# Optimization experiments

Measured on AMD Instinct MI355X. Metric: run time of the kernel, lower is better.

## Reference

```python
import jax, jax.numpy as jnp
import numpy as np
from jax import lax

B, S, TW = 16, 128, 16
VOCAB, EDIM = 50000, 300
NCHARS, CEDIM, CH = 100, 50, 50
HID = 256
NTAGS, MAXR = 10, 16
H2 = 2 * HID


def _lstm_dir(x, mask, wih, whh, b):
    # x: [N,T,D], mask: [N,T] bool. Returns masked outputs [N,T,H] and final hidden [N,H].
    Hd = whh.shape[1]
    Nn = x.shape[0]

    def step(carry, inp):
        h, c = carry
        xt, m = inp  # xt [N,D], m [N,1]
        z = xt @ wih.T + h @ whh.T + b
        i, f, g, o = jnp.split(z, 4, axis=-1)
        c_new = jax.nn.sigmoid(f) * c + jax.nn.sigmoid(i) * jnp.tanh(g)
        h_new = jax.nn.sigmoid(o) * jnp.tanh(c_new)
        c = jnp.where(m, c_new, c)
        h = jnp.where(m, h_new, h)
        return (h, c), jnp.where(m, h_new, 0.0)

    h0 = jnp.zeros((Nn, Hd), x.dtype)
    (hn, _), ys = lax.scan(step, (h0, h0), (x.transpose(1, 0, 2), mask.T[..., None]))
    return ys.transpose(1, 0, 2), hn


def _bilstm(x, lengths, pf, pb):
    # Mirrors pack_padded_sequence -> LSTM -> pad_packed (zeros past length).
    T = x.shape[1]
    mask = jnp.arange(T)[None, :] < lengths[:, None]
    yf, hf = _lstm_dir(x, mask, *pf)
    # per-sequence reversal for the backward direction
    idx = jnp.maximum(lengths[:, None] - 1 - jnp.arange(T)[None, :], 0)
    xr = jnp.take_along_axis(x, idx[:, :, None], axis=1)
    ybr, hb = _lstm_dir(xr, mask, *pb)
    yb = jnp.take_along_axis(ybr, idx[:, :, None], axis=1) * mask[:, :, None]
    return jnp.concatenate([yf, yb], -1), jnp.concatenate([hf, hb], -1)


def _forward(emb, char_emb, c_wih_f, c_whh_f, c_b_f, c_wih_b, c_whh_b, c_b_b,
             w_wih_f, w_whh_f, w_b_f, w_wih_b, w_whh_b, w_b_b, clf_w, clf_b,
             sentences, sentence_lengths, word_chars, word_lengths):
    word_repr = emb[sentences]  # [B,S,EDIM]
    # CharLSTM: final bi-hidden per word (all words of all sentences batched)
    cw = word_chars.reshape(B * S, TW)
    cl = word_lengths.reshape(B * S)
    ce = char_emb[cw]  # [B*S,TW,CEDIM]
    _, hn = _bilstm(ce, cl, (c_wih_f, c_whh_f, c_b_f), (c_wih_b, c_whh_b, c_b_b))
    sent_mask = jnp.arange(S)[None, :] < sentence_lengths[:, None]
    char_feat = hn.reshape(B, S, 2 * CH) * sent_mask[:, :, None]  # pad_sequence zeros
    x = jnp.concatenate([word_repr, char_feat], -1)  # [B,S,400]
    out, _ = _bilstm(x, sentence_lengths, (w_wih_f, w_whh_f, w_b_f), (w_wih_b, w_whh_b, w_b_b))
    u = out.transpose(1, 0, 2)  # [S,B,2H]  (unpacked.transpose(0,1))
    # prefix sums collapse the exhaustive sliding-window means into one pass
    csum = jnp.concatenate([jnp.zeros((1, B, H2), u.dtype), jnp.cumsum(u, axis=0)], 0)
    starts = np.concatenate([np.arange(0, S - r + 1) for r in range(1, MAXR + 1)])
    sizes = np.concatenate([np.full(S - r + 1, r) for r in range(1, MAXR + 1)])
    first = u[starts]                                   # [N,B,2H]
    last = u[starts + sizes - 1]                        # [N,B,2H]
    mean = (csum[starts + sizes] - csum[starts]) / jnp.asarray(sizes, u.dtype)[:, None, None]
    feats = jnp.concatenate([first, mean, last], -1)    # [N,B,6H]
    logits = jax.nn.relu(feats) @ clf_w.T + clf_b       # [N,B,NTAGS]
    return logits.transpose(1, 2, 0)                    # [B,NTAGS,N] (stack dim=-1)


def setup_inputs() -> dict:
    key = jax.random.key(0)
    ks = jax.random.split(key, 12)
    sc = 0.08

    def lstm_p(k, D, Hd):
        k1, k2, k3 = jax.random.split(k, 3)
        return (jax.random.normal(k1, (4 * Hd, D), jnp.float32) * sc,
                jax.random.normal(k2, (4 * Hd, Hd), jnp.float32) * sc,
                jax.random.normal(k3, (4 * Hd,), jnp.float32) * sc)

    emb = (jax.random.normal(ks[0], (VOCAB, EDIM), jnp.float32) * sc).at[0].set(0.0)
    char_emb = (jax.random.normal(ks[1], (NCHARS, CEDIM), jnp.float32) * sc).at[0].set(0.0)
    c_wih_f, c_whh_f, c_b_f = lstm_p(ks[2], CEDIM, CH)
    c_wih_b, c_whh_b, c_b_b = lstm_p(ks[3], CEDIM, CH)
    w_wih_f, w_whh_f, w_b_f = lstm_p(ks[4], EDIM + 2 * CH, HID)
    w_wih_b, w_whh_b, w_b_b = lstm_p(ks[5], EDIM + 2 * CH, HID)
    clf_w = jax.random.normal(ks[6], (NTAGS, 3 * H2), jnp.float32) * sc
    clf_b = jax.random.normal(ks[7], (NTAGS,), jnp.float32) * sc

    sentences = jax.random.randint(ks[8], (B, S), 1, VOCAB, jnp.int32)
    sl = jnp.sort(jax.random.randint(ks[9], (B,), S // 2, S + 1, jnp.int32))[::-1]
    sentence_lengths = sl.at[0].set(S)  # descending; max_len = S (static)
    word_chars = jax.random.randint(ks[10], (B, S, TW), 1, NCHARS, jnp.int32)
    word_lengths = jax.random.randint(ks[11], (B, S), 1, TW + 1, jnp.int32)

    return dict(emb=emb, char_emb=char_emb,
                c_wih_f=c_wih_f, c_whh_f=c_whh_f, c_b_f=c_b_f,
                c_wih_b=c_wih_b, c_whh_b=c_whh_b, c_b_b=c_b_b,
                w_wih_f=w_wih_f, w_whh_f=w_whh_f, w_b_f=w_b_f,
                w_wih_b=w_wih_b, w_whh_b=w_whh_b, w_b_b=w_b_b,
                clf_w=clf_w, clf_b=clf_b,
                sentences=sentences, sentence_lengths=sentence_lengths,
                word_chars=word_chars, word_lengths=word_lengths)


def reference(emb, char_emb, c_wih_f, c_whh_f, c_b_f, c_wih_b, c_whh_b, c_b_b,
              w_wih_f, w_whh_f, w_b_f, w_wih_b, w_whh_b, w_b_b, clf_w, clf_b,
              sentences, sentence_lengths, word_chars, word_lengths):
    return _forward(emb, char_emb, c_wih_f, c_whh_f, c_b_f, c_wih_b, c_whh_b, c_b_b,
                    w_wih_f, w_whh_f, w_b_f, w_wih_b, w_whh_b, w_b_b, clf_w, clf_b,
                    sentences, sentence_lengths, word_chars, word_lengths)
```

## Files before the change

kernel.cpp:

```cpp
#include <hip/hip_runtime.h>
#include <math.h>

typedef unsigned int u32;
typedef unsigned short u16;

#define NB 16
#define NS 128
#define NTW 16
#define NEDIM 300
#define NCED 50
#define NCH 50
#define NTAGS 10
#define XDIM 400
#define NWIN 1928

__device__ __forceinline__ float sigf(float x){ return 1.0f/(1.0f+expf(-x)); }
__device__ __forceinline__ u16 f2bu(float f){
  u32 u = __float_as_uint(f);
  return (u16)((u + 0x7fffu + ((u>>16)&1u))>>16);
}

__global__ void k_embed(const float* __restrict__ emb, const int* __restrict__ sent,
                        float* __restrict__ x){
  int n = blockIdx.x;
  int row = sent[n];
  const float* src = emb + (size_t)row*NEDIM;
  float* dst = x + (size_t)n*XDIM;
  for (int d = threadIdx.x; d < NEDIM; d += blockDim.x) dst[d] = src[d];
}

__global__ void k_char(const float* __restrict__ char_emb,
                       const float* __restrict__ wih_f, const float* __restrict__ whh_f, const float* __restrict__ b_f,
                       const float* __restrict__ wih_b, const float* __restrict__ whh_b, const float* __restrict__ b_b,
                       const int* __restrict__ wchars, const int* __restrict__ wlens,
                       const int* __restrict__ slens, float* __restrict__ x){
  const int dir = blockIdx.y;
  const int tid = threadIdx.x;
  __shared__ u16 wih_l[200*NCED];
  __shared__ u16 whh_l[200*NCED];
  __shared__ float z_l[200];
  __shared__ float h_l[NCH];
  const float* wih = dir ? wih_b : wih_f;
  const float* whh = dir ? whh_b : whh_f;
  const float* bp  = dir ? b_b   : b_f;
  for (int i = tid; i < 200*NCED; i += 256){
    wih_l[i] = f2bu(wih[i]);
    whh_l[i] = f2bu(whh[i]);
  }
  float bias = (tid < 200) ? bp[tid] : 0.f;
  __syncthreads();
  for (int w = 0; w < 4; ++w){
    int n = blockIdx.x*4 + w;
    int b = n >> 7, s = n & 127;
    int len = wlens[n];
    float c = 0.f, hcur = 0.f;
    if (tid < NCH) h_l[tid] = 0.f;
    __syncthreads();
    for (int t = 0; t < len; ++t){
      int tt = dir ? (len-1-t) : t;
      int ch = wchars[n*NTW + tt];
      if (tid < 200){
        const float* xe = char_emb + ch*NCED;
        const u16* wr = wih_l + tid*NCED;
        const u16* ur = whh_l + tid*NCED;
        float acc = bias;
        #pragma unroll 10
        for (int k = 0; k < NCED; ++k){
          float wv = __uint_as_float(((u32)wr[k])<<16);
          float uv = __uint_as_float(((u32)ur[k])<<16);
          acc += wv*xe[k] + uv*h_l[k];
        }
        z_l[tid] = acc;
      }
      __syncthreads();
      if (tid < NCH){
        float gi = sigf(z_l[tid]);
        float gf = sigf(z_l[NCH+tid]);
        float gg = tanhf(z_l[2*NCH+tid]);
        float go = sigf(z_l[3*NCH+tid]);
        c = gf*c + gi*gg;
        hcur = go*tanhf(c);
        h_l[tid] = hcur;
      }
      __syncthreads();
    }
    if (tid < NCH){
      float v = (s < slens[b]) ? hcur : 0.f;
      x[(size_t)n*XDIM + NEDIM + dir*NCH + tid] = v;
    }
  }
}

__global__ void k_wprep(const float* __restrict__ whh_f, const float* __restrict__ whh_b,
                        u32* __restrict__ whhT2){
  int gid = blockIdx.x*256 + threadIdx.x;
  int dir = gid >> 17;
  int rem = gid & 131071;
  int k2 = rem >> 10;
  int j  = rem & 1023;
  const float* src = dir ? whh_b : whh_f;
  u32 u0 = f2bu(src[j*256 + 2*k2]);
  u32 u1 = f2bu(src[j*256 + 2*k2 + 1]);
  whhT2[gid] = (u1<<16) | u0;
}

__global__ void k_wxg(const float* __restrict__ x,
                      const float* __restrict__ wih_f, const float* __restrict__ wih_b,
                      const float* __restrict__ bw_f, const float* __restrict__ bw_b,
                      float* __restrict__ xg){
  __shared__ float As[16][65];
  __shared__ float Bs[16][65];
  int tid = threadIdx.x;
  int tx = tid & 15, ty = tid >> 4;
  int n0 = blockIdx.x * 64;
  int m0 = blockIdx.y * 64;
  int dir = n0 >> 10;
  int j0  = n0 & 1023;
  const float* wih = dir ? wih_b : wih_f;
  const float* bw  = dir ? bw_b  : bw_f;
  float acc[4][4] = {};
  for (int k0 = 0; k0 < 400; k0 += 16){
    #pragma unroll
    for (int i = 0; i < 4; ++i){
      int e = tid + i*256;
      int kk = e & 15, m = e >> 4;
      As[kk][m] = x[(m0+m)*XDIM + k0 + kk];
      Bs[kk][m] = wih[(j0+m)*XDIM + k0 + kk];
    }
    __syncthreads();
    #pragma unroll
    for (int kk = 0; kk < 16; ++kk){
      float av[4], bv[4];
      #pragma unroll
      for (int i=0;i<4;++i) av[i] = As[kk][ty*4+i];
      #pragma unroll
      for (int j=0;j<4;++j) bv[j] = Bs[kk][tx*4+j];
      #pragma unroll
      for (int i=0;i<4;++i)
        #pragma unroll
        for (int j=0;j<4;++j) acc[i][j] = fmaf(av[i], bv[j], acc[i][j]);
    }
    __syncthreads();
  }
  #pragma unroll
  for (int i=0;i<4;++i){
    int m = m0 + ty*4 + i;
    #pragma unroll
    for (int j=0;j<4;++j){
      int jj = j0 + tx*4 + j;
      xg[dir*2097152 + m*1024 + jj] = acc[i][j] + bw[jj];
    }
  }
}

__global__ __launch_bounds__(512) void k_wlstm(const float* __restrict__ xg,
                        const u32* __restrict__ whhT2,
                        const int* __restrict__ slens, float* __restrict__ out){
  int b = blockIdx.x & 15, dir = blockIdx.x >> 4;
  int tid = threadIdx.x;
  int u = tid & 255, half = tid >> 8;
  __shared__ float h_l[256];
  __shared__ float part[1024];
  int len = slens[b];
  float c = 0.f;
  if (tid < 256) h_l[tid] = 0.f;
  __syncthreads();
  const float* xgb = xg + dir*2097152 + b*131072;
  const u32* W = whhT2 + dir*131072 + half*65536;
  const float* hb = h_l + half*128;
  for (int t = 0; t < len; ++t){
    int row = dir ? (len-1-t) : t;
    const float* xr = xgb + row*1024;
    float a0=0.f,a1=0.f,a2=0.f,a3=0.f;
    #pragma unroll 4
    for (int k2 = 0; k2 < 64; ++k2){
      u32 w0 = W[k2*1024 + u];
      u32 w1 = W[k2*1024 + 256 + u];
      u32 w2 = W[k2*1024 + 512 + u];
      u32 w3 = W[k2*1024 + 768 + u];
      float h0 = hb[2*k2], h1 = hb[2*k2+1];
      a0 = fmaf(h0, __uint_as_float(w0<<16), fmaf(h1, __uint_as_float(w0 & 0xffff0000u), a0));
      a1 = fmaf(h0, __uint_as_float(w1<<16), fmaf(h1, __uint_as_float(w1 & 0xffff0000u), a1));
      a2 = fmaf(h0, __uint_as_float(w2<<16), fmaf(h1, __uint_as_float(w2 & 0xffff0000u), a2));
      a3 = fmaf(h0, __uint_as_float(w3<<16), fmaf(h1, __uint_as_float(w3 & 0xffff0000u), a3));
    }
    if (half){ part[u]=a0; part[256+u]=a1; part[512+u]=a2; part[768+u]=a3; }
    __syncthreads();
    if (!half){
      a0 += part[u]     + xr[u];
      a1 += part[256+u] + xr[256+u];
      a2 += part[512+u] + xr[512+u];
      a3 += part[768+u] + xr[768+u];
      float gi=sigf(a0), gf=sigf(a1), gg=tanhf(a2), go=sigf(a3);
      c = gf*c + gi*gg;
      float hn = go*tanhf(c);
      h_l[u] = hn;
      out[(b*128+row)*512 + dir*256 + u] = hn;
    }
    __syncthreads();
  }
}

__global__ void k_csum(const float* __restrict__ out, float* __restrict__ csum){
  int gid = blockIdx.x*256 + threadIdx.x;
  int b = gid >> 9, d = gid & 511;
  float run = 0.f;
  csum[(b*129)*512 + d] = 0.f;
  for (int s = 0; s < 128; ++s){
    run += out[((b<<7)+s)*512 + d];
    csum[(b*129 + s + 1)*512 + d] = run;
  }
}

__global__ void k_ac(const float* __restrict__ out, const float* __restrict__ clf_w,
                     float* __restrict__ A, float* __restrict__ Cm){
  int gid = blockIdx.x*256 + threadIdx.x;
  int bs = gid / 10, tag = gid % 10;
  const float* o  = out + bs*512;
  const float* w1 = clf_w + tag*1536;
  const float* w3 = w1 + 1024;
  float a=0.f, cc=0.f;
  for (int d = 0; d < 512; ++d){
    float v = fmaxf(o[d], 0.f);
    a  = fmaf(v, w1[d], a);
    cc = fmaf(v, w3[d], cc);
  }
  A[gid] = a; Cm[gid] = cc;
}

__global__ void k_clf(const float* __restrict__ csum, const float* __restrict__ clf_w,
                      const float* __restrict__ clf_b, const float* __restrict__ A,
                      const float* __restrict__ Cm, float* __restrict__ dout){
  __shared__ float w2_l[NTAGS*512];
  int tid = threadIdx.x;
  for (int i = tid; i < NTAGS*512; i += 256){
    int tag = i >> 9, d = i & 511;
    w2_l[i] = clf_w[tag*1536 + 512 + d];
  }
  __syncthreads();
  int q = blockIdx.x*4 + (tid >> 6);
  int lane = tid & 63;
  int n = q >> 4, b = q & 15;
  int rem = n, r = 1;
  while (rem >= 129 - r){ rem -= 129 - r; ++r; }
  int s0 = rem, s1 = s0 + r - 1;
  float invr = 1.0f / (float)r;
  int d0 = lane*8;
  const float* c0 = csum + (b*129 + s0    )*512 + d0;
  const float* c1 = csum + (b*129 + s0 + r)*512 + d0;
  float m[8];
  #pragma unroll
  for (int i=0;i<8;++i) m[i] = fmaxf((c1[i]-c0[i])*invr, 0.f);
  float p[10];
  #pragma unroll
  for (int tag=0; tag<NTAGS; ++tag){
    const float* w = w2_l + tag*512 + d0;
    float s = 0.f;
    #pragma unroll
    for (int i=0;i<8;++i) s = fmaf(m[i], w[i], s);
    #pragma unroll
    for (int off=32; off>=1; off>>=1) s += __shfl_xor(s, off);
    p[tag] = s;
  }
  if (lane == 0){
    #pragma unroll
    for (int tag=0; tag<NTAGS; ++tag){
      float v = p[tag] + A[(b*128+s0)*10+tag] + Cm[(b*128+s1)*10+tag] + clf_b[tag];
      dout[b*(NTAGS*NWIN) + tag*NWIN + n] = v;
    }
  }
}

extern "C" void kernel_launch(void* const* d_in, const int* in_sizes, int n_in,
                              void* d_out, int out_size, void* d_ws, size_t ws_size,
                              hipStream_t stream){
  (void)in_sizes; (void)n_in; (void)out_size; (void)ws_size;
  const float* emb      = (const float*)d_in[0];
  const float* char_emb = (const float*)d_in[1];
  const float* c_wih_f  = (const float*)d_in[2];
  const float* c_whh_f  = (const float*)d_in[3];
  const float* c_b_f    = (const float*)d_in[4];
  const float* c_wih_b  = (const float*)d_in[5];
  const float* c_whh_b  = (const float*)d_in[6];
  const float* c_b_b    = (const float*)d_in[7];
  const float* w_wih_f  = (const float*)d_in[8];
  const float* w_whh_f  = (const float*)d_in[9];
  const float* w_b_f    = (const float*)d_in[10];
  const float* w_wih_b  = (const float*)d_in[11];
  const float* w_whh_b  = (const float*)d_in[12];
  const float* w_b_b    = (const float*)d_in[13];
  const float* clf_w    = (const float*)d_in[14];
  const float* clf_b    = (const float*)d_in[15];
  const int* sentences  = (const int*)d_in[16];
  const int* slens      = (const int*)d_in[17];
  const int* wchars     = (const int*)d_in[18];
  const int* wlens      = (const int*)d_in[19];

  float* ws   = (float*)d_ws;
  float* x    = ws;
  float* xg   = ws + 819200;
  float* outb = ws + 5013504;
  float* csum = ws + 6062080;
  float* A    = ws + 7118848;
  float* Cm   = ws + 7139328;
  u32*  whhT2 = (u32*)(ws + 7159808);

  hipMemsetAsync(outb, 0, (size_t)2048*512*sizeof(float), stream);
  k_embed<<<2048, 256, 0, stream>>>(emb, sentences, x);
  k_char<<<dim3(512,2), 256, 0, stream>>>(char_emb, c_wih_f, c_whh_f, c_b_f,
                                          c_wih_b, c_whh_b, c_b_b,
                                          wchars, wlens, slens, x);
  k_wprep<<<1024, 256, 0, stream>>>(w_whh_f, w_whh_b, whhT2);
  k_wxg<<<dim3(32,32), 256, 0, stream>>>(x, w_wih_f, w_wih_b, w_b_f, w_b_b, xg);
  k_wlstm<<<32, 512, 0, stream>>>(xg, whhT2, slens, outb);
  k_csum<<<32, 256, 0, stream>>>(outb, csum);
  k_ac<<<80, 256, 0, stream>>>(outb, clf_w, A, Cm);
  k_clf<<<7712, 256, 0, stream>>>(csum, clf_w, clf_b, A, Cm, (float*)d_out);
}
```

Baseline: 1.052 ms.

## Rewrite word BiLSTM recurrence as batched MFMA across two cooperating blocks

Result: faster. 899.3 us (-14.6%).

```diff
diff --git a/kernel.cpp b/kernel.cpp
--- a/kernel.cpp
+++ b/kernel.cpp
@@ -3,6 +3,9 @@
 
 typedef unsigned int u32;
 typedef unsigned short u16;
+typedef __attribute__((ext_vector_type(8))) short short8;
+typedef __attribute__((ext_vector_type(4))) float f32x4;
+typedef __attribute__((ext_vector_type(4))) u32 u32x4;
 
 #define NB 16
 #define NS 128
@@ -14,11 +17,16 @@
 #define XDIM 400
 #define NWIN 1928
 
-__device__ __forceinline__ float sigf(float x){ return 1.0f/(1.0f+expf(-x)); }
+__device__ __forceinline__ float sigf(float x){ return 1.0f/(1.0f+__expf(-x)); }
+__device__ __forceinline__ float tanhfast(float x){
+  float e = __expf(2.0f*x);
+  return 1.0f - 2.0f/(e + 1.0f);
+}
 __device__ __forceinline__ u16 f2bu(float f){
   u32 u = __float_as_uint(f);
   return (u16)((u + 0x7fffu + ((u>>16)&1u))>>16);
 }
+__device__ __forceinline__ float bf2f(u16 x){ return __uint_as_float(((u32)x)<<16); }
 
 __global__ void k_embed(const float* __restrict__ emb, const int* __restrict__ sent,
                         float* __restrict__ x){
@@ -91,23 +99,10 @@
   }
 }
 
-__global__ void k_wprep(const float* __restrict__ whh_f, const float* __restrict__ whh_b,
-                        u32* __restrict__ whhT2){
-  int gid = blockIdx.x*256 + threadIdx.x;
-  int dir = gid >> 17;
-  int rem = gid & 131071;
-  int k2 = rem >> 10;
-  int j  = rem & 1023;
-  const float* src = dir ? whh_b : whh_f;
-  u32 u0 = f2bu(src[j*256 + 2*k2]);
-  u32 u1 = f2bu(src[j*256 + 2*k2 + 1]);
-  whhT2[gid] = (u1<<16) | u0;
-}
-
 __global__ void k_wxg(const float* __restrict__ x,
                       const float* __restrict__ wih_f, const float* __restrict__ wih_b,
                       const float* __restrict__ bw_f, const float* __restrict__ bw_b,
-                      float* __restrict__ xg){
+                      u16* __restrict__ xgb){
   __shared__ float As[16][65];
   __shared__ float Bs[16][65];
   int tid = threadIdx.x;
@@ -148,56 +143,166 @@
     #pragma unroll
     for (int j=0;j<4;++j){
       int jj = j0 + tx*4 + j;
-      xg[dir*2097152 + m*1024 + jj] = acc[i][j] + bw[jj];
-    }
-  }
-}
-
-__global__ __launch_bounds__(512) void k_wlstm(const float* __restrict__ xg,
-                        const u32* __restrict__ whhT2,
-                        const int* __restrict__ slens, float* __restrict__ out){
-  int b = blockIdx.x & 15, dir = blockIdx.x >> 4;
-  int tid = threadIdx.x;
-  int u = tid & 255, half = tid >> 8;
-  __shared__ float h_l[256];
-  __shared__ float part[1024];
-  int len = slens[b];
-  float c = 0.f;
-  if (tid < 256) h_l[tid] = 0.f;
+      xgb[(size_t)dir*2097152 + m*1024 + jj] = f2bu(acc[i][j] + bw[jj]);
+    }
+  }
+}
+
+__global__ __launch_bounds__(1024, 4) void k_wlstm2(
+    const float* __restrict__ whh_f, const float* __restrict__ whh_b,
+    const u16* __restrict__ xgB, const int* __restrict__ slens,
+    float* __restrict__ out, u32* __restrict__ xh, int* __restrict__ flags){
+  const int dir  = blockIdx.x >> 1;
+  const int half = blockIdx.x & 1;
+  const int tid  = threadIdx.x;
+  const int lane = tid & 63;
+  const int w    = tid >> 6;
+  const int q    = lane >> 4;
+  const int jc   = lane & 15;
+
+  __shared__ __align__(16) u16  Hbuf[2][16*256];
+  __shared__ __align__(16) float abuf[32][64][4];
+  __shared__ __align__(16) u16  xstg[2][16*512];
+
+  const float* whh = dir ? whh_b : whh_f;
+
+  const int v = w & 7, rsel = w >> 3;
+  const int b0c = q*4 + 2*rsel, b1c = b0c + 1;
+  const int len0 = slens[b0c], len1 = slens[b1c];
+  const int len_s = slens[w];
+
+  short8 Bf[2][8];
+  #pragma unroll
+  for (int l = 0; l < 2; ++l){
+    int jt = w*2 + l;
+    int g = jt >> 3, vv = jt & 7;
+    int j = g*256 + half*128 + vv*16 + jc;
+    const float* wr = whh + (size_t)j*256;
+    #pragma unroll
+    for (int kc = 0; kc < 8; ++kc){
+      int k0 = kc*32 + q*8;
+      f32x4 w0 = *(const f32x4*)(wr + k0);
+      f32x4 w1 = *(const f32x4*)(wr + k0 + 4);
+      short8 s;
+      s[0]=(short)f2bu(w0[0]); s[1]=(short)f2bu(w0[1]);
+      s[2]=(short)f2bu(w0[2]); s[3]=(short)f2bu(w0[3]);
+      s[4]=(short)f2bu(w1[0]); s[5]=(short)f2bu(w1[1]);
+      s[6]=(short)f2bu(w1[2]); s[7]=(short)f2bu(w1[3]);
+      Bf[l][kc] = s;
+    }
+  }
+
+  for (int i = tid; i < 2048; i += 1024) ((u32*)Hbuf[0])[i] = 0u;
+
+  {
+    int rowS = dir ? (len_s - 1) : 0;
+    const u16* src = xgB + ((size_t)dir<<21) + ((w*128 + rowS)*1024 + q*256 + half*128 + jc*8);
+    u32x4 d = *(const u32x4*)src;
+    *(u32x4*)&xstg[0][(w*4 + q)*128 + jc*8] = d;
+  }
   __syncthreads();
-  const float* xgb = xg + dir*2097152 + b*131072;
-  const u32* W = whhT2 + dir*131072 + half*65536;
-  const float* hb = h_l + half*128;
-  for (int t = 0; t < len; ++t){
-    int row = dir ? (len-1-t) : t;
-    const float* xr = xgb + row*1024;
-    float a0=0.f,a1=0.f,a2=0.f,a3=0.f;
-    #pragma unroll 4
-    for (int k2 = 0; k2 < 64; ++k2){
-      u32 w0 = W[k2*1024 + u];
-      u32 w1 = W[k2*1024 + 256 + u];
-      u32 w2 = W[k2*1024 + 512 + u];
-      u32 w3 = W[k2*1024 + 768 + u];
-      float h0 = hb[2*k2], h1 = hb[2*k2+1];
-      a0 = fmaf(h0, __uint_as_float(w0<<16), fmaf(h1, __uint_as_float(w0 & 0xffff0000u), a0));
-      a1 = fmaf(h0, __uint_as_float(w1<<16), fmaf(h1, __uint_as_float(w1 & 0xffff0000u), a1));
-      a2 = fmaf(h0, __uint_as_float(w2<<16), fmaf(h1, __uint_as_float(w2 & 0xffff0000u), a2));
-      a3 = fmaf(h0, __uint_as_float(w3<<16), fmaf(h1, __uint_as_float(w3 & 0xffff0000u), a3));
-    }
-    if (half){ part[u]=a0; part[256+u]=a1; part[512+u]=a2; part[768+u]=a3; }
-    __syncthreads();
-    if (!half){
-      a0 += part[u]     + xr[u];
-      a1 += part[256+u] + xr[256+u];
-      a2 += part[512+u] + xr[512+u];
-      a3 += part[768+u] + xr[768+u];
-      float gi=sigf(a0), gf=sigf(a1), gg=tanhf(a2), go=sigf(a3);
-      c = gf*c + gi*gg;
-      float hn = go*tanhf(c);
-      h_l[u] = hn;
-      out[(b*128+row)*512 + dir*256 + u] = hn;
-    }
-    __syncthreads();
+
+  const int fl_idx = dir*2 + half;
+  const int fl_p   = dir*2 + (1 - half);
+  u32* xh_own = xh + fl_idx*2048;
+  u32* xh_par = xh + fl_p*2048;
+
+  float c0 = 0.f, c1 = 0.f, h0 = 0.f, h1 = 0.f;
+  int cur = 0;
+
+  for (int t = 0; t < 128; ++t){
+    u32x4 stg;
+    const bool do_stage = (t < 127);
+    if (do_stage){
+      int rowS = dir ? (len_s - 2 - t) : (t + 1);
+      rowS = rowS < 0 ? 0 : rowS;
+      const u16* src = xgB + ((size_t)dir<<21) + ((w*128 + rowS)*1024 + q*256 + half*128 + jc*8);
+      stg = *(const u32x4*)src;
+    }
+
+    f32x4 acc0 = {0.f,0.f,0.f,0.f};
+    f32x4 acc1 = {0.f,0.f,0.f,0.f};
+    {
+      const char* Hc = (const char*)Hbuf[cur];
+      int arow = jc;
+      #pragma unroll
+      for (int kc = 0; kc < 8; ++kc){
+        int kb = (kc*64 + q*16) ^ ((arow & 7) << 4);
+        short8 af = *(const short8*)(Hc + arow*512 + kb);
+        acc0 = __builtin_amdgcn_mfma_f32_16x16x32_bf16(af, Bf[0][kc], acc0, 0, 0, 0);
+        acc1 = __builtin_amdgcn_mfma_f32_16x16x32_bf16(af, Bf[1][kc], acc1, 0, 0, 0);
+      }
+    }
+    *(f32x4*)&abuf[w*2  ][lane][0] = acc0;
+    *(f32x4*)&abuf[w*2+1][lane][0] = acc1;
+    __syncthreads();
+
+    int nxt = cur ^ 1;
+    {
+      f32x4 zi = *(const f32x4*)&abuf[0*8+v][lane][0];
+      f32x4 zf = *(const f32x4*)&abuf[1*8+v][lane][0];
+      f32x4 zg = *(const f32x4*)&abuf[2*8+v][lane][0];
+      f32x4 zo = *(const f32x4*)&abuf[3*8+v][lane][0];
+      const u16* xs = xstg[t & 1];
+      const int ucol = v*16 + jc;
+      const int ug   = half*128 + ucol;
+
+      float Zi0 = (rsel ? zi[2] : zi[0]) + bf2f(xs[(b0c*4+0)*128 + ucol]);
+      float Zf0 = (rsel ? zf[2] : zf[0]) + bf2f(xs[(b0c*4+1)*128 + ucol]);
+      float Zg0 = (rsel ? zg[2] : zg[0]) + bf2f(xs[(b0c*4+2)*128 + ucol]);
+      float Zo0 = (rsel ? zo[2] : zo[0]) + bf2f(xs[(b0c*4+3)*128 + ucol]);
+      if (t < len0){
+        float gi = sigf(Zi0), gf = sigf(Zf0), gg = tanhfast(Zg0), go = sigf(Zo0);
+        c0 = gf*c0 + gi*gg;
+        h0 = go*tanhfast(c0);
+        int row = dir ? (len0-1-t) : t;
+        out[((b0c<<7)+row)*512 + dir*256 + ug] = h0;
+      }
+      float Zi1 = (rsel ? zi[3] : zi[1]) + bf2f(xs[(b1c*4+0)*128 + ucol]);
+      float Zf1 = (rsel ? zf[3] : zf[1]) + bf2f(xs[(b1c*4+1)*128 + ucol]);
+      float Zg1 = (rsel ? zg[3] : zg[1]) + bf2f(xs[(b1c*4+2)*128 + ucol]);
+      float Zo1 = (rsel ? zo[3] : zo[1]) + bf2f(xs[(b1c*4+3)*128 + ucol]);
+      if (t < len1){
+        float gi = sigf(Zi1), gf = sigf(Zf1), gg = tanhfast(Zg1), go = sigf(Zo1);
+        c1 = gf*c1 + gi*gg;
+        h1 = go*tanhfast(c1);
+        int row = dir ? (len1-1-t) : t;
+        out[((b1c<<7)+row)*512 + dir*256 + ug] = h1;
+      }
+      u16 hb0 = f2bu(h0), hb1 = f2bu(h1);
+      Hbuf[nxt][b0c*256 + ((((ug*2) ^ ((b0c&7)<<4))) >> 1)] = hb0;
+      Hbuf[nxt][b1c*256 + ((((ug*2) ^ ((b1c&7)<<4))) >> 1)] = hb1;
+      u32 pack = ((u32)hb1 << 16) | (u32)hb0;
+      __hip_atomic_store(&xh_own[(t&1)*1024 + ucol*8 + q*2 + rsel], pack,
+                         __ATOMIC_RELAXED, __HIP_MEMORY_SCOPE_AGENT);
+    }
+    __syncthreads();
+
+    if (tid == 0){
+      __hip_atomic_store(&flags[fl_idx], t+1, __ATOMIC_RELEASE, __HIP_MEMORY_SCOPE_AGENT);
+      int spins = 0;
+      while (__hip_atomic_load(&flags[fl_p], __ATOMIC_ACQUIRE, __HIP_MEMORY_SCOPE_AGENT) < t+1){
+        __builtin_amdgcn_s_sleep(2);
+        if (++spins > (1<<16)) break;
+      }
+    }
+    __syncthreads();
+
+    {
+      u32 d = __hip_atomic_load(&xh_par[(t&1)*1024 + tid],
+                                __ATOMIC_RELAXED, __HIP_MEMORY_SCOPE_AGENT);
+      int ul  = tid >> 3;
+      int qq  = (tid >> 1) & 3, rs = tid & 1;
+      int bb0 = qq*4 + rs*2, bb1 = bb0 + 1;
+      int ugp = (1-half)*128 + ul;
+      Hbuf[nxt][bb0*256 + ((((ugp*2) ^ ((bb0&7)<<4))) >> 1)] = (u16)(d & 0xffffu);
+      Hbuf[nxt][bb1*256 + ((((ugp*2) ^ ((bb1&7)<<4))) >> 1)] = (u16)(d >> 16);
+    }
+    if (do_stage){
+      *(u32x4*)&xstg[(t+1)&1][(w*4 + q)*128 + jc*8] = stg;
+    }
+    __syncthreads();
+    cur = nxt;
   }
 }
 
@@ -221,9 +326,9 @@
   const float* w3 = w1 + 1024;
   float a=0.f, cc=0.f;
   for (int d = 0; d < 512; ++d){
-    float v = fmaxf(o[d], 0.f);
-    a  = fmaf(v, w1[d], a);
-    cc = fmaf(v, w3[d], cc);
+    float vv = fmaxf(o[d], 0.f);
+    a  = fmaf(vv, w1[d], a);
+    cc = fmaf(vv, w3[d], cc);
   }
   A[gid] = a; Cm[gid] = cc;
 }
@@ -238,9 +343,9 @@
     w2_l[i] = clf_w[tag*1536 + 512 + d];
   }
   __syncthreads();
-  int q = blockIdx.x*4 + (tid >> 6);
+  int qq = blockIdx.x*4 + (tid >> 6);
   int lane = tid & 63;
-  int n = q >> 4, b = q & 15;
+  int n = qq >> 4, b = qq & 15;
   int rem = n, r = 1;
   while (rem >= 129 - r){ rem -= 129 - r; ++r; }
   int s0 = rem, s1 = s0 + r - 1;
@@ -254,10 +359,10 @@
   float p[10];
   #pragma unroll
   for (int tag=0; tag<NTAGS; ++tag){
-    const float* w = w2_l + tag*512 + d0;
+    const float* wv = w2_l + tag*512 + d0;
     float s = 0.f;
     #pragma unroll
-    for (int i=0;i<8;++i) s = fmaf(m[i], w[i], s);
+    for (int i=0;i<8;++i) s = fmaf(m[i], wv[i], s);
     #pragma unroll
     for (int off=32; off>=1; off>>=1) s += __shfl_xor(s, off);
     p[tag] = s;
@@ -265,8 +370,8 @@
   if (lane == 0){
     #pragma unroll
     for (int tag=0; tag<NTAGS; ++tag){
-      float v = p[tag] + A[(b*128+s0)*10+tag] + Cm[(b*128+s1)*10+tag] + clf_b[tag];
-      dout[b*(NTAGS*NWIN) + tag*NWIN + n] = v;
+      float vv = p[tag] + A[(b*128+s0)*10+tag] + Cm[(b*128+s1)*10+tag] + clf_b[tag];
+      dout[b*(NTAGS*NWIN) + tag*NWIN + n] = vv;
     }
   }
 }
@@ -298,21 +403,22 @@
 
   float* ws   = (float*)d_ws;
   float* x    = ws;
-  float* xg   = ws + 819200;
-  float* outb = ws + 5013504;
-  float* csum = ws + 6062080;
-  float* A    = ws + 7118848;
-  float* Cm   = ws + 7139328;
-  u32*  whhT2 = (u32*)(ws + 7159808);
+  u16*  xgb   = (u16*)(ws + 819200);
+  float* outb = ws + 2916352;
+  float* csum = ws + 3964928;
+  float* A    = ws + 5021696;
+  float* Cm   = ws + 5042176;
+  u32*  xh    = (u32*)(ws + 5062656);
+  int*  flags = (int*)(ws + 5070848);
 
   hipMemsetAsync(outb, 0, (size_t)2048*512*sizeof(float), stream);
+  hipMemsetAsync(flags, 0, 256, stream);
   k_embed<<<2048, 256, 0, stream>>>(emb, sentences, x);
   k_char<<<dim3(512,2), 256, 0, stream>>>(char_emb, c_wih_f, c_whh_f, c_b_f,
                                           c_wih_b, c_whh_b, c_b_b,
                                           wchars, wlens, slens, x);
-  k_wprep<<<1024, 256, 0, stream>>>(w_whh_f, w_whh_b, whhT2);
-  k_wxg<<<dim3(32,32), 256, 0, stream>>>(x, w_wih_f, w_wih_b, w_b_f, w_b_b, xg);
-  k_wlstm<<<32, 512, 0, stream>>>(xg, whhT2, slens, outb);
+  k_wxg<<<dim3(32,32), 256, 0, stream>>>(x, w_wih_f, w_wih_b, w_b_f, w_b_b, xgb);
+  k_wlstm2<<<4, 1024, 0, stream>>>(w_whh_f, w_whh_b, xgb, slens, outb, xh, flags);
   k_csum<<<32, 256, 0, stream>>>(outb, csum);
   k_ac<<<80, 256, 0, stream>>>(outb, clf_w, A, Cm);
   k_clf<<<7712, 256, 0, stream>>>(csum, clf_w, clf_b, A, Cm, (float*)d_out);
```
